# Kernel optimization log

Hardware: AMD Instinct MI355X
Metric: run time of the kernel (lower is better)

The kernel has to match this reference:

```python
import jax, jax.numpy as jnp
import numpy as np

B, S, ENC_D, DEC_D, ATTN_D, OUT_D = 32, 2048, 1024, 1024, 1024, 1024
SCALING = 1.0


def setup_inputs() -> dict:
    key = jax.random.key(0)
    ks = jax.random.split(key, 10)
    enc_states = jax.random.normal(ks[0], (B, S, ENC_D), dtype=jnp.float32)
    # lengths in [S//2, S] so every row has at least one valid position
    enc_len = jax.random.randint(ks[1], (B,), S // 2, S + 1, dtype=jnp.int32)
    dec_states = jax.random.normal(ks[2], (B, DEC_D), dtype=jnp.float32)
    s = 0.02
    W_enc = jax.random.normal(ks[3], (ENC_D, ATTN_D), dtype=jnp.float32) * s
    b_enc = jnp.zeros((ATTN_D,), dtype=jnp.float32)
    W_dec = jax.random.normal(ks[4], (DEC_D, ATTN_D), dtype=jnp.float32) * s
    b_dec = jnp.zeros((ATTN_D,), dtype=jnp.float32)
    w_attn = jax.random.normal(ks[5], (ATTN_D,), dtype=jnp.float32) * s
    W_out = jax.random.normal(ks[6], (ENC_D, OUT_D), dtype=jnp.float32) * s
    b_out = jnp.zeros((OUT_D,), dtype=jnp.float32)
    return {
        "enc_states": enc_states,
        "dec_states": dec_states,
        "W_enc": W_enc, "b_enc": b_enc,
        "W_dec": W_dec, "b_dec": b_dec,
        "w_attn": w_attn,
        "W_out": W_out, "b_out": b_out,
        "enc_len": enc_len,
    }


def reference(enc_states, dec_states, W_enc, b_enc, W_dec, b_dec, w_attn, W_out, b_out, enc_len):
    # precomputed_enc_h = mlp_enc(enc_states): [B, S, ATTN_D]
    enc_h = jnp.einsum("bse,ea->bsa", enc_states, W_enc) + b_enc
    # dec_h = mlp_dec(dec_states): [B, ATTN_D]
    dec_h = dec_states @ W_dec + b_dec
    # additive (Bahdanau) score: tanh(enc_h + dec_h) . w_attn -> [B, S]
    attn = jnp.einsum("bsa,a->bs", jnp.tanh(enc_h + dec_h[:, None, :]), w_attn)
    # length mask
    mask = jnp.arange(enc_states.shape[1])[None, :] < enc_len[:, None]  # [B, S]
    attn = jnp.where(mask, attn, -jnp.inf)
    attn = jax.nn.softmax(attn * SCALING, axis=-1)
    # context = attn @ enc_states -> [B, ENC_D]
    context = jnp.einsum("bs,bse->be", attn, enc_states)
    context = context @ W_out + b_out
    return (context, attn)
```

## Files before the change

kernel.cpp:

```cpp
#include <hip/hip_runtime.h>
#include <cstdint>
#include <cstddef>

#define BATCH 32
#define SEQ   2048
#define DIM   1024
#define MROWS (BATCH*SEQ)

typedef __attribute__((ext_vector_type(4))) float  floatx4;
typedef __attribute__((ext_vector_type(8))) short  short8;

__device__ __forceinline__ unsigned short f2bf(float f) {
  unsigned int u = __float_as_uint(f);
  u += 0x7fffu + ((u >> 16) & 1u);
  return (unsigned short)(u >> 16);
}

__device__ __forceinline__ void async16(const void* g, void* l) {
  __builtin_amdgcn_global_load_lds(
      (const __attribute__((address_space(1))) unsigned int*)g,
      (__attribute__((address_space(3))) unsigned int*)l, 16, 0, 0);
}

__device__ __forceinline__ float fast_tanh(float x) {
  float e = __expf(2.0f * x);
  return 1.0f - 2.0f * __builtin_amdgcn_rcpf(1.0f + e);
}

__global__ void k_convert(const float* __restrict__ enc, const int* __restrict__ enc_len,
                          unsigned short* __restrict__ Abf) {
  int b = blockIdx.y;
  int r0 = blockIdx.x * 8;
  if (r0 >= enc_len[b]) return;
  size_t base = ((size_t)b * SEQ + r0) * DIM;
  const float4* src = (const float4*)(enc + base);
  ushort4* dst = (ushort4*)(Abf + base);
  int tid = threadIdx.x;
#pragma unroll
  for (int i = 0; i < 8; ++i) {
    float4 v = src[tid + i * 256];
    ushort4 h;
    h.x = f2bf(v.x); h.y = f2bf(v.y); h.z = f2bf(v.z); h.w = f2bf(v.w);
    dst[tid + i * 256] = h;
  }
}

__global__ void k_transpose(const float* __restrict__ W, unsigned short* __restrict__ Wt) {
  __shared__ float tile[32][33];
  int n0 = blockIdx.x * 32, k0 = blockIdx.y * 32;
  int tx = threadIdx.x, ty = threadIdx.y;
#pragma unroll
  for (int i = 0; i < 4; ++i) {
    int y = ty + i * 8;
    tile[y][tx] = W[(size_t)(k0 + y) * DIM + n0 + tx];
  }
  __syncthreads();
#pragma unroll
  for (int i = 0; i < 4; ++i) {
    int y = ty + i * 8;
    Wt[(size_t)(n0 + y) * DIM + k0 + tx] = f2bf(tile[tx][y]);
  }
}

__global__ void k_dech(const float* __restrict__ dec, const float* __restrict__ W_dec,
                       const float* __restrict__ b_dec, const float* __restrict__ b_enc,
                       float* __restrict__ dech) {
  int b = blockIdx.y, z = blockIdx.z;
  int a = blockIdx.x * 256 + threadIdx.x;
  float acc = (z == 0) ? (b_dec[a] + b_enc[a]) : 0.0f;
  const float* dr = dec + (size_t)b * DIM + z * 128;
  const float* wc = W_dec + (size_t)z * 128 * DIM + a;
#pragma unroll 8
  for (int e = 0; e < 128; ++e)
    acc = fmaf(dr[e], wc[(size_t)e * DIM], acc);
  atomicAdd(&dech[(size_t)b * DIM + a], acc);
}

#define PH_BAR do { asm volatile("" ::: "memory"); __builtin_amdgcn_s_barrier(); asm volatile("" ::: "memory"); } while(0)
#define SCHED0 __builtin_amdgcn_sched_barrier(0)
#define SP1 __builtin_amdgcn_s_setprio(1)
#define SP0 __builtin_amdgcn_s_setprio(0)
#define VMCNT(n) asm volatile("s_waitcnt vmcnt(" #n ")" ::: "memory")

__global__ void __launch_bounds__(512, 2) k_gemm256(
    const unsigned short* __restrict__ Abf,
    const unsigned short* __restrict__ Wt,
    const float* __restrict__ dech,
    const float* __restrict__ w_attn,
    const int* __restrict__ enc_len,
    float* __restrict__ score)
{
  int bid = blockIdx.x;
  int t  = (bid & 7) * 128 + (bid >> 3);
  int nb = t & 3;
  int rt = t >> 2;
  int bb = rt >> 3;
  int len = enc_len[bb];
  if (((rt & 7) * 256) >= len) return;

  __shared__ __align__(16) char lds[131072];

  int tid = threadIdx.x;
  int w = tid >> 6, lane = tid & 63;
  int wr = w >> 2;
  int wc = w & 3;
  int li = lane & 15, g = lane >> 4;
  int xl = (li & 7) << 4;

  const char* Ag = (const char*)(Abf + (size_t)rt * 256 * DIM);
  const char* Bg = (const char*)(Wt  + (size_t)nb * 256 * DIM);

  size_t soff[2][2];
  int    ldso[2][2];
#pragma unroll
  for (int h = 0; h < 2; ++h)
#pragma unroll
    for (int i = 0; i < 2; ++i) {
      int P = h * 16384 + (w * 2 + i) * 1024 + lane * 16;
      int L = P ^ (((P >> 7) & 7) << 4);
      soff[h][i] = (size_t)(L >> 7) * (DIM * 2) + (L & 127);
      ldso[h][i] = h * 16384 + (w * 2 + i) * 1024;
    }

#define STAGE_A(buf, h, kt) do { \
  async16(Ag + soff[h][0] + (size_t)(kt) * 128, lds + (buf) * 32768 + ldso[h][0]); \
  async16(Ag + soff[h][1] + (size_t)(kt) * 128, lds + (buf) * 32768 + ldso[h][1]); \
} while (0)
#define STAGE_B(buf, h, kt) do { \
  async16(Bg + soff[h][0] + (size_t)(kt) * 128, lds + 65536 + (buf) * 32768 + ldso[h][0]); \
  async16(Bg + soff[h][1] + (size_t)(kt) * 128, lds + 65536 + (buf) * 32768 + ldso[h][1]); \
} while (0)

  short8 aF[4][2];
  short8 bF[2][2][2];
  floatx4 acc[8][4] = {};

#define READ_A(buf, mh) do { \
  const char* base_ = lds + (buf) * 32768 + (wr * 128 + (mh) * 64 + li) * 128; \
  int c0_ = (g * 16) ^ xl; \
  _Pragma("unroll") for (int tmq = 0; tmq < 4; ++tmq) { \
    aF[tmq][0] = *(const short8*)(base_ + tmq * 2048 + c0_); \
    aF[tmq][1] = *(const short8*)(base_ + tmq * 2048 + (c0_ ^ 64)); \
  } \
} while (0)
#define READ_B(buf, nh) do { \
  const char* base_ = lds + 65536 + (buf) * 32768 + (wc * 64 + (nh) * 32 + li) * 128; \
  int c0_ = (g * 16) ^ xl; \
  _Pragma("unroll") for (int tnq = 0; tnq < 2; ++tnq) { \
    bF[nh][tnq][0] = *(const short8*)(base_ + tnq * 2048 + c0_); \
    bF[nh][tnq][1] = *(const short8*)(base_ + tnq * 2048 + (c0_ ^ 64)); \
  } \
} while (0)
#define MFMA_Q(mh, nh) do { \
  _Pragma("unroll") for (int ks = 0; ks < 2; ++ks) \
  _Pragma("unroll") for (int tmq = 0; tmq < 4; ++tmq) \
  _Pragma("unroll") for (int tnq = 0; tnq < 2; ++tnq) \
    acc[(mh) * 4 + tmq][(nh) * 2 + tnq] = __builtin_amdgcn_mfma_f32_16x16x32_bf16( \
        aF[tmq][ks], bF[nh][tnq][ks], acc[(mh) * 4 + tmq][(nh) * 2 + tnq], 0, 0, 0); \
} while (0)

#define TILE_STEP(CUR, KT2, MODE) do { \
   \
  READ_A(CUR, 0); \
  READ_B(CUR, 0); \
  PH_BAR; SCHED0; SP1; MFMA_Q(0, 0); SP0; SCHED0; \
  PH_BAR; \
   \
  READ_B(CUR, 1); \
  PH_BAR; SCHED0; SP1; MFMA_Q(0, 1); SP0; SCHED0; \
  PH_BAR; \
   \
  READ_A(CUR, 1); \
  if ((MODE) == 0) { STAGE_B(CUR, 0, KT2); STAGE_B(CUR, 1, KT2); } \
  PH_BAR; SCHED0; SP1; MFMA_Q(1, 1); SP0; SCHED0; \
  PH_BAR; \
   \
  if ((MODE) == 0) { STAGE_A(CUR, 0, KT2); STAGE_A(CUR, 1, KT2); } \
  PH_BAR; SCHED0; SP1; MFMA_Q(1, 0); SP0; SCHED0; \
  if ((MODE) == 0) { VMCNT(8); } else if ((MODE) == 1) { VMCNT(0); } \
  PH_BAR; \
} while (0)

  STAGE_B(0, 0, 0); STAGE_B(0, 1, 0); STAGE_A(0, 0, 0); STAGE_A(0, 1, 0);
  STAGE_B(1, 0, 1); STAGE_B(1, 1, 1); STAGE_A(1, 0, 1); STAGE_A(1, 1, 1);
  VMCNT(8);
  PH_BAR;

#pragma unroll 1
  for (int u = 0; u < 14; u += 2) {
    TILE_STEP(0, u + 2, 0);
    TILE_STEP(1, u + 3, 0);
  }
  TILE_STEP(0, 0, 1);
  TILE_STEP(1, 0, 2);

  float dh[4], wa[4];
#pragma unroll
  for (int tn = 0; tn < 4; ++tn) {
    int n = nb * 256 + wc * 64 + tn * 16 + li;
    dh[tn] = dech[(size_t)bb * DIM + n];
    wa[tn] = w_attn[n];
  }
#pragma unroll
  for (int tm = 0; tm < 8; ++tm) {
    int mrow = rt * 256 + wr * 128 + tm * 16 + g * 4;
#pragma unroll
    for (int r = 0; r < 4; ++r) {
      float v = 0.0f;
#pragma unroll
      for (int tn = 0; tn < 4; ++tn)
        v = fmaf(wa[tn], fast_tanh(acc[tm][tn][r] + dh[tn]), v);
      v += __shfl_xor(v, 1);
      v += __shfl_xor(v, 2);
      v += __shfl_xor(v, 4);
      v += __shfl_xor(v, 8);
      if (li == 0) atomicAdd(&score[mrow + r], v);
    }
  }
#undef TILE_STEP
#undef MFMA_Q
#undef READ_B
#undef READ_A
#undef STAGE_B
#undef STAGE_A
}

__global__ void __launch_bounds__(256, 2) k_gemm_f32(
    const float* __restrict__ A, const unsigned short* __restrict__ Wt,
    const float* __restrict__ dech, const float* __restrict__ w_attn,
    const int* __restrict__ enc_len, float* __restrict__ score)
{
  int linear = blockIdx.x;
  int xcd = linear & 7;
  int j   = linear >> 3;
  int rb  = xcd * 64 + (j >> 3);
  int nb  = j & 7;
  int bb  = rb >> 4;
  int len = enc_len[bb];
  if (((rb & 15) * 128) >= len) return;

  __shared__ __align__(16) unsigned short sA[128 * 40];
  __shared__ __align__(16) unsigned short sB[128 * 32];

  int tid  = threadIdx.x;
  int w    = tid >> 6, lane = tid & 63;
  int wm   = (w >> 1) * 64, wn = (w & 1) * 64;
  int li   = lane & 15, g = lane >> 4;

  const float*          Abase = A  + (size_t)rb * 128 * DIM;
  const unsigned short* Bbase = Wt + (size_t)nb * 128 * DIM;

  floatx4 acc[4][4] = {};

  for (int kb = 0; kb < 32; ++kb) {
    __syncthreads();
#pragma unroll
    for (int i = 0; i < 2; ++i) {
      int c  = (w * 2 + i) * 64 + lane;
      int n  = c >> 2;
      int kh = (c & 3) ^ ((n >> 1) & 3);
      async16(Bbase + (size_t)n * DIM + kb * 32 + kh * 8, (char*)sB + (w * 2 + i) * 1024);
    }
#pragma unroll
    for (int i = 0; i < 4; ++i) {
      int f4  = tid + i * 256;
      int row = f4 >> 3, kq = f4 & 7;
      float4 v = *(const float4*)(Abase + (size_t)row * DIM + kb * 32 + kq * 4);
      ushort4 h;
      h.x = f2bf(v.x); h.y = f2bf(v.y); h.z = f2bf(v.z); h.w = f2bf(v.w);
      *(ushort4*)&sA[row * 40 + kq * 4] = h;
    }
    __syncthreads();

    short8 af[4], bfr[4];
#pragma unroll
    for (int t = 0; t < 4; ++t) {
      int row = wm + t * 16 + li;
      af[t] = *(const short8*)&sA[row * 40 + g * 8];
      int nl = wn + t * 16 + li;
      int phys = (nl << 2) | (g ^ ((nl >> 1) & 3));
      bfr[t] = *(const short8*)((const char*)sB + phys * 16);
    }
#pragma unroll
    for (int tm = 0; tm < 4; ++tm)
#pragma unroll
      for (int tn = 0; tn < 4; ++tn)
        acc[tm][tn] = __builtin_amdgcn_mfma_f32_16x16x32_bf16(af[tm], bfr[tn], acc[tm][tn], 0, 0, 0);
  }

  float dh[4], wa[4];
#pragma unroll
  for (int tn = 0; tn < 4; ++tn) {
    int n = nb * 128 + wn + tn * 16 + li;
    dh[tn] = dech[(size_t)bb * DIM + n];
    wa[tn] = w_attn[n];
  }
#pragma unroll
  for (int tm = 0; tm < 4; ++tm) {
    int mrow = rb * 128 + wm + tm * 16 + g * 4;
#pragma unroll
    for (int r = 0; r < 4; ++r) {
      float v = 0.0f;
#pragma unroll
      for (int tn = 0; tn < 4; ++tn)
        v = fmaf(wa[tn], fast_tanh(acc[tm][tn][r] + dh[tn]), v);
      v += __shfl_xor(v, 1);
      v += __shfl_xor(v, 2);
      v += __shfl_xor(v, 4);
      v += __shfl_xor(v, 8);
      if (li == 0) atomicAdd(&score[mrow + r], v);
    }
  }
}

__global__ void k_softmax(const float* __restrict__ score, const int* __restrict__ enc_len,
                          float* __restrict__ attn) {
  int b = blockIdx.x, tid = threadIdx.x;
  int len = enc_len[b];
  __shared__ float red[256];
  float v[8];
  float m = -1e30f;
#pragma unroll
  for (int i = 0; i < 8; ++i) {
    int s = tid + i * 256;
    v[i] = score[(size_t)b * SEQ + s];
    if (s < len) m = fmaxf(m, v[i]);
  }
  red[tid] = m; __syncthreads();
  for (int st = 128; st > 0; st >>= 1) {
    if (tid < st) red[tid] = fmaxf(red[tid], red[tid + st]);
    __syncthreads();
  }
  float mx = red[0]; __syncthreads();
  float sum = 0.0f;
#pragma unroll
  for (int i = 0; i < 8; ++i) {
    int s = tid + i * 256;
    float e = (s < len) ? __expf(v[i] - mx) : 0.0f;
    v[i] = e; sum += e;
  }
  red[tid] = sum; __syncthreads();
  for (int st = 128; st > 0; st >>= 1) {
    if (tid < st) red[tid] += red[tid + st];
    __syncthreads();
  }
  float inv = 1.0f / red[0];
#pragma unroll
  for (int i = 0; i < 8; ++i)
    attn[(size_t)b * SEQ + tid + i * 256] = v[i] * inv;
}

__global__ void k_context(const float* __restrict__ enc, const float* __restrict__ attn,
                          const int* __restrict__ enc_len, float* __restrict__ ctx) {
  int b = blockIdx.y, sc = blockIdx.x;
  int len = enc_len[b];
  int s0 = sc * 32;
  if (s0 >= len) return;
  int cnt = min(32, len - s0);
  int tid = threadIdx.x;
  const float* base = enc + ((size_t)b * SEQ + s0) * DIM + tid * 4;
  const float* ap   = attn + (size_t)b * SEQ + s0;
  float a0 = 0.f, a1 = 0.f, a2 = 0.f, a3 = 0.f;
  int i = 0;
  for (; i + 8 <= cnt; i += 8) {
    float4 x[8];
    float  w[8];
#pragma unroll
    for (int u = 0; u < 8; ++u)
      x[u] = *(const float4*)(base + (size_t)(i + u) * DIM);
#pragma unroll
    for (int u = 0; u < 8; ++u)
      w[u] = ap[i + u];
#pragma unroll
    for (int u = 0; u < 8; ++u) {
      a0 = fmaf(w[u], x[u].x, a0); a1 = fmaf(w[u], x[u].y, a1);
      a2 = fmaf(w[u], x[u].z, a2); a3 = fmaf(w[u], x[u].w, a3);
    }
  }
  for (; i < cnt; ++i) {
    float w = ap[i];
    float4 x = *(const float4*)(base + (size_t)i * DIM);
    a0 = fmaf(w, x.x, a0); a1 = fmaf(w, x.y, a1);
    a2 = fmaf(w, x.z, a2); a3 = fmaf(w, x.w, a3);
  }
  float* c = ctx + (size_t)b * DIM + tid * 4;
  atomicAdd(c + 0, a0); atomicAdd(c + 1, a1);
  atomicAdd(c + 2, a2); atomicAdd(c + 3, a3);
}

__global__ void k_out(const float* __restrict__ ctx, const float* __restrict__ W_out,
                      const float* __restrict__ b_out, float* __restrict__ out) {
  int b = blockIdx.y, z = blockIdx.z;
  int o = blockIdx.x * 256 + threadIdx.x;
  float acc = (z == 0) ? b_out[o] : 0.0f;
  const float* cr = ctx + (size_t)b * DIM + z * 128;
  const float* wc = W_out + (size_t)z * 128 * DIM + o;
#pragma unroll 8
  for (int e = 0; e < 128; ++e)
    acc = fmaf(cr[e], wc[(size_t)e * DIM], acc);
  atomicAdd(&out[(size_t)b * DIM + o], acc);
}

extern "C" void kernel_launch(void* const* d_in, const int* in_sizes, int n_in,
                              void* d_out, int out_size, void* d_ws, size_t ws_size,
                              hipStream_t stream) {
  (void)in_sizes; (void)n_in; (void)out_size;
  const float* enc_states = (const float*)d_in[0];
  const float* dec_states = (const float*)d_in[1];
  const float* W_enc      = (const float*)d_in[2];
  const float* b_enc      = (const float*)d_in[3];
  const float* W_dec      = (const float*)d_in[4];
  const float* b_dec      = (const float*)d_in[5];
  const float* w_attn     = (const float*)d_in[6];
  const float* W_out      = (const float*)d_in[7];
  const float* b_out      = (const float*)d_in[8];
  const int*   enc_len    = (const int*)  d_in[9];

  float* out_ctx  = (float*)d_out;
  float* out_attn = (float*)d_out + BATCH * DIM;

  char* ws = (char*)d_ws;
  unsigned short* Wt  = (unsigned short*)ws;
  float* score = (float*)(ws + (2u << 20));
  float* ctx   = (float*)(ws + (2u << 20) + 262144);
  float* dech  = (float*)(ws + (2u << 20) + 262144 + 131072);
  unsigned short* Abf = (unsigned short*)(ws + (3u << 20));
  const bool fast = ws_size >= ((size_t)(3u << 20) + ((size_t)MROWS * DIM * 2));

  hipMemsetAsync(ws + (2u << 20), 0, 262144 + 131072 + 131072, stream);
  hipMemsetAsync(d_out, 0, (size_t)BATCH * DIM * sizeof(float), stream);

  k_transpose<<<dim3(32, 32), dim3(32, 8), 0, stream>>>(W_enc, Wt);
  k_dech<<<dim3(4, BATCH, 8), 256, 0, stream>>>(dec_states, W_dec, b_dec, b_enc, dech);
  if (fast) {
    k_convert<<<dim3(SEQ / 8, BATCH), 256, 0, stream>>>(enc_states, enc_len, Abf);
    k_gemm256<<<1024, 512, 0, stream>>>(Abf, Wt, dech, w_attn, enc_len, score);
  } else {
    k_gemm_f32<<<4096, 256, 0, stream>>>(enc_states, Wt, dech, w_attn, enc_len, score);
  }
  k_softmax<<<BATCH, 256, 0, stream>>>(score, enc_len, out_attn);
  k_context<<<dim3(64, BATCH), 256, 0, stream>>>(enc_states, out_attn, enc_len, ctx);
  k_out<<<dim3(4, BATCH, 8), 256, 0, stream>>>(ctx, W_out, b_out, out_ctx);
}
```

Baseline: 603.0 us.

## Prefetch next-tile A fragments in GEMM, batch 8 rows per thread in small GEMVs

The main bf16 GEMM loop now splits A fragment reads into 2-row groups and reads the first A fragment of the next buffer before the last MFMA quarter of the current step. This lets LDS reads overlap with MFMA work across tile steps, and the staging address math is simplified to a shared base plus offsets. The small dec/out GEMV kernels now have each thread handle 8 batch rows, so each weight load is reused eight times and the grid is smaller. In exchange, register pressure rises and the GEMV kernels launch fewer blocks.

```diff
diff --git a/kernel.cpp b/kernel.cpp
--- a/kernel.cpp
+++ b/kernel.cpp
@@ -65,15 +65,24 @@
 __global__ void k_dech(const float* __restrict__ dec, const float* __restrict__ W_dec,
                        const float* __restrict__ b_dec, const float* __restrict__ b_enc,
                        float* __restrict__ dech) {
-  int b = blockIdx.y, z = blockIdx.z;
-  int a = blockIdx.x * 256 + threadIdx.x;
-  float acc = (z == 0) ? (b_dec[a] + b_enc[a]) : 0.0f;
-  const float* dr = dec + (size_t)b * DIM + z * 128;
+  int a  = blockIdx.x * 256 + threadIdx.x;
+  int bg = blockIdx.y * 8;
+  int z  = blockIdx.z;
+  float bias = (z == 0) ? (b_dec[a] + b_enc[a]) : 0.0f;
+  float acc[8];
+#pragma unroll
+  for (int j = 0; j < 8; ++j) acc[j] = bias;
   const float* wc = W_dec + (size_t)z * 128 * DIM + a;
-#pragma unroll 8
-  for (int e = 0; e < 128; ++e)
-    acc = fmaf(dr[e], wc[(size_t)e * DIM], acc);
-  atomicAdd(&dech[(size_t)b * DIM + a], acc);
+#pragma unroll 4
+  for (int e = 0; e < 128; ++e) {
+    float w = wc[(size_t)e * DIM];
+#pragma unroll
+    for (int j = 0; j < 8; ++j)
+      acc[j] = fmaf(dec[(size_t)(bg + j) * DIM + z * 128 + e], w, acc[j]);
+  }
+#pragma unroll
+  for (int j = 0; j < 8; ++j)
+    atomicAdd(&dech[(size_t)(bg + j) * DIM + a], acc[j]);
 }
 
 #define PH_BAR do { asm volatile("" ::: "memory"); __builtin_amdgcn_s_barrier(); asm volatile("" ::: "memory"); } while(0)
@@ -110,74 +119,76 @@
   const char* Ag = (const char*)(Abf + (size_t)rt * 256 * DIM);
   const char* Bg = (const char*)(Wt  + (size_t)nb * 256 * DIM);
 
-  size_t soff[2][2];
-  int    ldso[2][2];
-#pragma unroll
-  for (int h = 0; h < 2; ++h)
-#pragma unroll
-    for (int i = 0; i < 2; ++i) {
-      int P = h * 16384 + (w * 2 + i) * 1024 + lane * 16;
-      int L = P ^ (((P >> 7) & 7) << 4);
-      soff[h][i] = (size_t)(L >> 7) * (DIM * 2) + (L & 127);
-      ldso[h][i] = h * 16384 + (w * 2 + i) * 1024;
-    }
+  size_t sbase = (size_t)((lane >> 3) * 2048 +
+                 (((lane & 7) << 4) ^ (((lane >> 3) & 7) << 4)));
+  size_t swoff = (size_t)(w * 2) * 16384;
+  int    ldbase = w * 2048;
 
 #define STAGE_A(buf, h, kt) do { \
-  async16(Ag + soff[h][0] + (size_t)(kt) * 128, lds + (buf) * 32768 + ldso[h][0]); \
-  async16(Ag + soff[h][1] + (size_t)(kt) * 128, lds + (buf) * 32768 + ldso[h][1]); \
+  async16(Ag + sbase + swoff + (size_t)(h) * 262144 + (size_t)(kt) * 128, \
+          lds + (buf) * 32768 + ldbase + (h) * 16384); \
+  async16(Ag + sbase + swoff + 16384 + (size_t)(h) * 262144 + (size_t)(kt) * 128, \
+          lds + (buf) * 32768 + ldbase + 1024 + (h) * 16384); \
 } while (0)
 #define STAGE_B(buf, h, kt) do { \
-  async16(Bg + soff[h][0] + (size_t)(kt) * 128, lds + 65536 + (buf) * 32768 + ldso[h][0]); \
-  async16(Bg + soff[h][1] + (size_t)(kt) * 128, lds + 65536 + (buf) * 32768 + ldso[h][1]); \
-} while (0)
-
-  short8 aF[4][2];
-  short8 bF[2][2][2];
+  async16(Bg + sbase + swoff + (size_t)(h) * 262144 + (size_t)(kt) * 128, \
+          lds + 65536 + (buf) * 32768 + ldbase + (h) * 16384); \
+  async16(Bg + sbase + swoff + 16384 + (size_t)(h) * 262144 + (size_t)(kt) * 128, \
+          lds + 65536 + (buf) * 32768 + ldbase + 1024 + (h) * 16384); \
+} while (0)
+
+  short8 sA0[2][2], sA1[2][2];
+  short8 aX[2][2];
+  short8 bX[2][2];
   floatx4 acc[8][4] = {};
 
-#define READ_A(buf, mh) do { \
-  const char* base_ = lds + (buf) * 32768 + (wr * 128 + (mh) * 64 + li) * 128; \
+#define RD_A2(buf, f0, DST) do { \
+  const char* base_ = lds + (buf) * 32768 + (wr * 128 + (f0) * 16 + li) * 128; \
   int c0_ = (g * 16) ^ xl; \
-  _Pragma("unroll") for (int tmq = 0; tmq < 4; ++tmq) { \
-    aF[tmq][0] = *(const short8*)(base_ + tmq * 2048 + c0_); \
-    aF[tmq][1] = *(const short8*)(base_ + tmq * 2048 + (c0_ ^ 64)); \
+  _Pragma("unroll") for (int j = 0; j < 2; ++j) { \
+    DST[j][0] = *(const short8*)(base_ + j * 2048 + c0_); \
+    DST[j][1] = *(const short8*)(base_ + j * 2048 + (c0_ ^ 64)); \
   } \
 } while (0)
-#define READ_B(buf, nh) do { \
+#define RD_B(buf, nh, DST) do { \
   const char* base_ = lds + 65536 + (buf) * 32768 + (wc * 64 + (nh) * 32 + li) * 128; \
   int c0_ = (g * 16) ^ xl; \
   _Pragma("unroll") for (int tnq = 0; tnq < 2; ++tnq) { \
-    bF[nh][tnq][0] = *(const short8*)(base_ + tnq * 2048 + c0_); \
-    bF[nh][tnq][1] = *(const short8*)(base_ + tnq * 2048 + (c0_ ^ 64)); \
+    DST[tnq][0] = *(const short8*)(base_ + tnq * 2048 + c0_); \
+    DST[tnq][1] = *(const short8*)(base_ + tnq * 2048 + (c0_ ^ 64)); \
   } \
 } while (0)
-#define MFMA_Q(mh, nh) do { \
+#define MFMA_Q(mh, nh, ALO, AHI, BB) do { \
   _Pragma("unroll") for (int ks = 0; ks < 2; ++ks) \
-  _Pragma("unroll") for (int tmq = 0; tmq < 4; ++tmq) \
-  _Pragma("unroll") for (int tnq = 0; tnq < 2; ++tnq) \
-    acc[(mh) * 4 + tmq][(nh) * 2 + tnq] = __builtin_amdgcn_mfma_f32_16x16x32_bf16( \
-        aF[tmq][ks], bF[nh][tnq][ks], acc[(mh) * 4 + tmq][(nh) * 2 + tnq], 0, 0, 0); \
-} while (0)
-
-#define TILE_STEP(CUR, KT2, MODE) do { \
+  _Pragma("unroll") for (int tnq = 0; tnq < 2; ++tnq) { \
+    acc[(mh)*4+0][(nh)*2+tnq] = __builtin_amdgcn_mfma_f32_16x16x32_bf16(ALO[0][ks], BB[tnq][ks], acc[(mh)*4+0][(nh)*2+tnq], 0, 0, 0); \
+    acc[(mh)*4+1][(nh)*2+tnq] = __builtin_amdgcn_mfma_f32_16x16x32_bf16(ALO[1][ks], BB[tnq][ks], acc[(mh)*4+1][(nh)*2+tnq], 0, 0, 0); \
+    acc[(mh)*4+2][(nh)*2+tnq] = __builtin_amdgcn_mfma_f32_16x16x32_bf16(AHI[0][ks], BB[tnq][ks], acc[(mh)*4+2][(nh)*2+tnq], 0, 0, 0); \
+    acc[(mh)*4+3][(nh)*2+tnq] = __builtin_amdgcn_mfma_f32_16x16x32_bf16(AHI[1][ks], BB[tnq][ks], acc[(mh)*4+3][(nh)*2+tnq], 0, 0, 0); \
+  } \
+} while (0)
+
+#define TILE_STEP(CUR, KT2, MODE, SP_, SQ_) do { \
    \
-  READ_A(CUR, 0); \
-  READ_B(CUR, 0); \
-  PH_BAR; SCHED0; SP1; MFMA_Q(0, 0); SP0; SCHED0; \
+  RD_A2(CUR, 2, aX); \
+  RD_B(CUR, 0, bX); \
+  PH_BAR; SCHED0; SP1; MFMA_Q(0, 0, SP_, aX, bX); SP0; SCHED0; \
   PH_BAR; \
    \
-  READ_B(CUR, 1); \
-  PH_BAR; SCHED0; SP1; MFMA_Q(0, 1); SP0; SCHED0; \
+  RD_B(CUR, 1, SQ_); \
+  PH_BAR; SCHED0; SP1; MFMA_Q(0, 1, SP_, aX, SQ_); SP0; SCHED0; \
   PH_BAR; \
    \
-  READ_A(CUR, 1); \
   if ((MODE) == 0) { STAGE_B(CUR, 0, KT2); STAGE_B(CUR, 1, KT2); } \
-  PH_BAR; SCHED0; SP1; MFMA_Q(1, 1); SP0; SCHED0; \
+  RD_A2(CUR, 4, SP_); \
+  RD_A2(CUR, 6, aX); \
+  PH_BAR; SCHED0; SP1; MFMA_Q(1, 1, SP_, aX, SQ_); SP0; SCHED0; \
   PH_BAR; \
    \
   if ((MODE) == 0) { STAGE_A(CUR, 0, KT2); STAGE_A(CUR, 1, KT2); } \
-  PH_BAR; SCHED0; SP1; MFMA_Q(1, 0); SP0; SCHED0; \
   if ((MODE) == 0) { VMCNT(8); } else if ((MODE) == 1) { VMCNT(0); } \
+  if ((MODE) < 2) RD_A2((CUR) ^ 1, 0, SQ_); \
+  PH_BAR; SCHED0; SP1; MFMA_Q(1, 0, SP_, aX, bX); SP0; SCHED0; \
   PH_BAR; \
 } while (0)
 
@@ -185,14 +196,15 @@
   STAGE_B(1, 0, 1); STAGE_B(1, 1, 1); STAGE_A(1, 0, 1); STAGE_A(1, 1, 1);
   VMCNT(8);
   PH_BAR;
+  RD_A2(0, 0, sA0);
 
 #pragma unroll 1
   for (int u = 0; u < 14; u += 2) {
-    TILE_STEP(0, u + 2, 0);
-    TILE_STEP(1, u + 3, 0);
-  }
-  TILE_STEP(0, 0, 1);
-  TILE_STEP(1, 0, 2);
+    TILE_STEP(0, u + 2, 0, sA0, sA1);
+    TILE_STEP(1, u + 3, 0, sA1, sA0);
+  }
+  TILE_STEP(0, 0, 1, sA0, sA1);
+  TILE_STEP(1, 0, 2, sA1, sA0);
 
   float dh[4], wa[4];
 #pragma unroll
@@ -219,8 +231,8 @@
   }
 #undef TILE_STEP
 #undef MFMA_Q
-#undef READ_B
-#undef READ_A
+#undef RD_B
+#undef RD_A2
 #undef STAGE_B
 #undef STAGE_A
 }
@@ -390,15 +402,24 @@
 
 __global__ void k_out(const float* __restrict__ ctx, const float* __restrict__ W_out,
                       const float* __restrict__ b_out, float* __restrict__ out) {
-  int b = blockIdx.y, z = blockIdx.z;
-  int o = blockIdx.x * 256 + threadIdx.x;
-  float acc = (z == 0) ? b_out[o] : 0.0f;
-  const float* cr = ctx + (size_t)b * DIM + z * 128;
+  int o  = blockIdx.x * 256 + threadIdx.x;
+  int bg = blockIdx.y * 8;
+  int z  = blockIdx.z;
+  float bias = (z == 0) ? b_out[o] : 0.0f;
+  float acc[8];
+#pragma unroll
+  for (int j = 0; j < 8; ++j) acc[j] = bias;
   const float* wc = W_out + (size_t)z * 128 * DIM + o;
-#pragma unroll 8
-  for (int e = 0; e < 128; ++e)
-    acc = fmaf(cr[e], wc[(size_t)e * DIM], acc);
-  atomicAdd(&out[(size_t)b * DIM + o], acc);
+#pragma unroll 4
+  for (int e = 0; e < 128; ++e) {
+    float w = wc[(size_t)e * DIM];
+#pragma unroll
+    for (int j = 0; j < 8; ++j)
+      acc[j] = fmaf(ctx[(size_t)(bg + j) * DIM + z * 128 + e], w, acc[j]);
+  }
+#pragma unroll
+  for (int j = 0; j < 8; ++j)
+    atomicAdd(&out[(size_t)(bg + j) * DIM + o], acc[j]);
 }
 
 extern "C" void kernel_launch(void* const* d_in, const int* in_sizes, int n_in,
@@ -431,7 +452,7 @@
   hipMemsetAsync(d_out, 0, (size_t)BATCH * DIM * sizeof(float), stream);
 
   k_transpose<<<dim3(32, 32), dim3(32, 8), 0, stream>>>(W_enc, Wt);
-  k_dech<<<dim3(4, BATCH, 8), 256, 0, stream>>>(dec_states, W_dec, b_dec, b_enc, dech);
+  k_dech<<<dim3(4, 4, 8), 256, 0, stream>>>(dec_states, W_dec, b_dec, b_enc, dech);
   if (fast) {
     k_convert<<<dim3(SEQ / 8, BATCH), 256, 0, stream>>>(enc_states, enc_len, Abf);
     k_gemm256<<<1024, 512, 0, stream>>>(Abf, Wt, dech, w_attn, enc_len, score);
@@ -440,5 +461,5 @@
   }
   k_softmax<<<BATCH, 256, 0, stream>>>(score, enc_len, out_attn);
   k_context<<<dim3(64, BATCH), 256, 0, stream>>>(enc_states, out_attn, enc_len, ctx);
-  k_out<<<dim3(4, BATCH, 8), 256, 0, stream>>>(ctx, W_out, b_out, out_ctx);
-}
+  k_out<<<dim3(4, 4, 8), 256, 0, stream>>>(ctx, W_out, b_out, out_ctx);
+}
```

New measurement: 611.8 us. About the same (+1.5%).
